# Kernel optimization log

Hardware: AMD Instinct MI355X
Metric: run time of the kernel (lower is better)

## Reference

```python
import jax, jax.numpy as jnp
import numpy as np

B, NPG, K, F_IN, H = 64, 256, 100, 5, 128  # graphs, nodes/graph, knn k, in feats, hidden
N = B * NPG
H2 = 6 * H
SLOPE = 0.01  # leaky_relu default
EPS = 1e-5    # batchnorm eps


def _leaky(x):
    return jnp.where(x > 0, x, SLOPE * x)


def _knn_edges(x):
    # knn_graph(x, K, batch), loop=False, flow=source_to_target: edges j->i for the
    # K nearest neighbors j of node i within the same graph.
    xb = x.reshape(B, NPG, F_IN)
    d2 = jnp.sum((xb[:, :, None, :] - xb[:, None, :, :]) ** 2, axis=-1)  # [B,NPG,NPG]
    d2 = d2 + jnp.eye(NPG, dtype=d2.dtype) * 1e10  # exclude self
    _, idx = jax.lax.top_k(-d2, K)  # [B,NPG,K] local neighbor ids
    offs = (jnp.arange(B) * NPG)[:, None, None]
    src = (idx + offs).reshape(-1)
    dst = jnp.broadcast_to(jnp.arange(NPG)[None, :, None] + offs, (B, NPG, K)).reshape(-1)
    return src, dst


def _tagconv(x, src, dst, norm, Ws, b):
    # PyG TAGConv: out = sum_k lin_k(L^k x), L = D^-1/2 A D^-1/2 (no self loops)
    out = x @ Ws[0]
    h = x
    for k in range(1, Ws.shape[0]):
        msg = h[src] * norm[:, None]                      # gather [E,F]
        h = jax.ops.segment_sum(msg, dst, num_segments=N)  # scatter-add
        out = out + h @ Ws[k]
    return out + b


def _pool(x, batch):
    cnt = jax.ops.segment_sum(jnp.ones((N,), x.dtype), batch, num_segments=B)
    mean = jax.ops.segment_sum(x, batch, num_segments=B) / cnt[:, None]
    mx = jax.ops.segment_max(x, batch, num_segments=B)
    return jnp.concatenate([mean, mx], axis=1)  # [B, 2F]


def reference(x, batch, conv1_w, conv1_b, conv2_w, conv2_b, conv3_w, conv3_b,
              bn_gamma, bn_beta, lin_w, lin_b, out_w, out_b):
    src, dst = _knn_edges(x)
    # gcn_norm: deg from target side, symmetric scaling
    deg = jax.ops.segment_sum(jnp.ones(src.shape, x.dtype), dst, num_segments=N)
    dinv = jnp.where(deg > 0, deg ** -0.5, 0.0)
    norm = dinv[src] * dinv[dst]

    h = _leaky(_tagconv(x, src, dst, norm, conv1_w, conv1_b))
    p1 = _pool(h, batch)
    h = _leaky(_tagconv(h, src, dst, norm, conv2_w, conv2_b))
    p2 = _pool(h, batch)
    h = _leaky(_tagconv(h, src, dst, norm, conv3_w, conv3_b))
    p3 = _pool(h, batch)

    g = jnp.concatenate([p1, p2, p3], axis=1)  # [B, 768]
    mu = jnp.mean(g, axis=0)
    var = jnp.mean((g - mu) ** 2, axis=0)
    g = (g - mu) * jax.lax.rsqrt(var + EPS) * bn_gamma + bn_beta

    for i in range(5):
        g = _leaky(g @ lin_w[i] + lin_b[i])
    return (g @ out_w + out_b).reshape(-1)


def setup_inputs() -> dict:
    key = jax.random.key(0)
    ks = jax.random.split(key, 16)
    x = jax.random.normal(ks[0], (N, F_IN), jnp.float32)
    batch = jnp.repeat(jnp.arange(B, dtype=jnp.int32), NPG)

    def w(k, shape, fan_in):
        return jax.random.normal(k, shape, jnp.float32) * (1.0 / np.sqrt(fan_in))

    return {
        "x": x, "batch": batch,
        "conv1_w": w(ks[1], (3, F_IN, H), F_IN), "conv1_b": jnp.zeros((H,), jnp.float32),
        "conv2_w": w(ks[2], (3, H, H), H), "conv2_b": jnp.zeros((H,), jnp.float32),
        "conv3_w": w(ks[3], (3, H, H), H), "conv3_b": jnp.zeros((H,), jnp.float32),
        "bn_gamma": jnp.ones((H2,), jnp.float32), "bn_beta": jnp.zeros((H2,), jnp.float32),
        "lin_w": w(ks[4], (5, H2, H2), H2), "lin_b": jnp.zeros((5, H2), jnp.float32),
        "out_w": w(ks[5], (H2, 1), H2), "out_b": jnp.zeros((1,), jnp.float32),
    }
```

## Files before the change

kernel.cpp:

```cpp
#include <hip/hip_runtime.h>
#include <hip/hip_bf16.h>
#include <math.h>

#define NN 16384
#define BB 64
#define NPG 256
#define KNN 100
#define FIN 5
#define HH 128
#define H2 768
#define SLOPE 0.01f

typedef __bf16 bf16x8 __attribute__((ext_vector_type(8)));
typedef float f32x4 __attribute__((ext_vector_type(4)));

__device__ __forceinline__ int detect_bf(const void* gamma) {
    return ((const unsigned*)gamma)[0] == 0x3F803F80u;
}
__device__ __forceinline__ float loadin(const void* p, size_t i, int bf) {
    return bf ? __bfloat162float(((const __hip_bfloat16*)p)[i]) : ((const float*)p)[i];
}
template <typename T>
__device__ __forceinline__ float ldT(const T* p, size_t i) { return (float)p[i]; }
template <>
__device__ __forceinline__ float ldT<__hip_bfloat16>(const __hip_bfloat16* p, size_t i) {
    return __bfloat162float(p[i]);
}
__device__ __forceinline__ float4 ldT4(const float* p) { return *(const float4*)p; }
__device__ __forceinline__ float4 ldT4(const __hip_bfloat16* p) {
    ushort4 u = *(const ushort4*)p;
    return make_float4(__uint_as_float((unsigned)u.x << 16),
                       __uint_as_float((unsigned)u.y << 16),
                       __uint_as_float((unsigned)u.z << 16),
                       __uint_as_float((unsigned)u.w << 16));
}
__device__ __forceinline__ void stage_chunk(float* dst, const float* src, int n, int t) {
    const float4* s = (const float4*)src;
    float4* d = (float4*)dst;
    int n4 = n >> 2;
    for (int i = t; i < n4; i += 256) d[i] = s[i];
}
__device__ __forceinline__ void stage_chunk(float* dst, const __hip_bfloat16* src, int n, int t) {
    const ushort4* s = (const ushort4*)src;
    int n4 = n >> 2;
    for (int i = t; i < n4; i += 256) {
        ushort4 u = s[i];
        dst[i * 4 + 0] = __uint_as_float((unsigned)u.x << 16);
        dst[i * 4 + 1] = __uint_as_float((unsigned)u.y << 16);
        dst[i * 4 + 2] = __uint_as_float((unsigned)u.z << 16);
        dst[i * 4 + 3] = __uint_as_float((unsigned)u.w << 16);
    }
}

__device__ __forceinline__ unsigned enc_f(float f) {
    unsigned u = __float_as_uint(f);
    return (u & 0x80000000u) ? ~u : (u | 0x80000000u);
}
__device__ __forceinline__ float dec_f(unsigned u) {
    return __uint_as_float((u & 0x80000000u) ? (u & 0x7FFFFFFFu) : ~u);
}
__device__ __forceinline__ unsigned f2bf(float f) {
    unsigned u = __float_as_uint(f);
    unsigned r = 0x7fffu + ((u >> 16) & 1u);
    return (u + r) >> 16;
}
__device__ __forceinline__ void split1(float x, unsigned short& h, unsigned short& l) {
    unsigned u = __float_as_uint(x);
    unsigned hb = u & 0xFFFF0000u;
    h = (unsigned short)(hb >> 16);
    float rem = x - __uint_as_float(hb);
    l = (unsigned short)f2bf(rem);
}

__global__ __launch_bounds__(256) void knn_kernel(const void* __restrict__ x_in,
                                                  const void* gamma,
                                                  unsigned char* __restrict__ nbr,
                                                  float* __restrict__ g,
                                                  float* __restrict__ outf,
                                                  unsigned* __restrict__ done) {
    int blk = blockIdx.x;
    int bf = detect_bf(gamma);
    int b = blk >> 6;
    int wave = threadIdx.x >> 6;
    int lane = threadIdx.x & 63;
    int il = ((blk & 63) << 2) + wave;
    {
        int gi = blk * 256 + threadIdx.x;
        if (blk < 192 && gi < BB * H2) {
            int cm = gi & 255;
            g[gi] = (cm < 128) ? 0.0f : __uint_as_float(0x007FFFFFu);
        }
        if (blk == 0 && threadIdx.x < BB) {
            outf[threadIdx.x] = 0.0f;
            done[threadIdx.x] = 0u;
        }
    }
    __shared__ float xg[FIN * NPG];
    for (int idx = threadIdx.x; idx < NPG * FIN; idx += 256) {
        int node = idx / FIN, c = idx - node * FIN;
        xg[c * NPG + node] = loadin(x_in, (size_t)b * NPG * FIN + idx, bf);
    }
    __syncthreads();
    float dq[4] = {0.f, 0.f, 0.f, 0.f};
    #pragma unroll
    for (int c = 0; c < FIN; ++c) {
        float xi = xg[c * NPG + il];
        float4 xv = *(const float4*)&xg[c * NPG + lane * 4];
        float d0 = xi - xv.x, d1 = xi - xv.y, d2 = xi - xv.z, d3 = xi - xv.w;
        dq[0] += d0 * d0; dq[1] += d1 * d1; dq[2] += d2 * d2; dq[3] += d3 * d3;
    }
    unsigned dk[4];
    #pragma unroll
    for (int q = 0; q < 4; ++q) {
        int e = lane * 4 + q;
        float dd = (e == il) ? 1e30f : dq[q];
        dk[q] = __float_as_uint(dd);
    }
    unsigned P = 0;
    for (int bit = 30; bit >= 0; --bit) {
        unsigned cand = P | (1u << bit);
        int c = __popcll(__ballot(dk[0] < cand)) + __popcll(__ballot(dk[1] < cand))
              + __popcll(__ballot(dk[2] < cand)) + __popcll(__ballot(dk[3] < cand));
        if (c < KNN) P = cand;
    }
    unsigned long long meq[4];
    int n_less = 0;
    #pragma unroll
    for (int q = 0; q < 4; ++q) {
        n_less += __popcll(__ballot(dk[q] < P));
        meq[q] = __ballot(dk[q] == P);
    }
    int quota = KNN - n_less;
    unsigned long long below = (1ull << lane) - 1ull;
    int run_eq = __popcll(meq[0] & below) + __popcll(meq[1] & below)
               + __popcll(meq[2] & below) + __popcll(meq[3] & below);
    bool sel[4];
    #pragma unroll
    for (int q = 0; q < 4; ++q) {
        int iseq = (int)((meq[q] >> lane) & 1ull);
        sel[q] = (dk[q] < P) || (iseq && run_eq < quota);
        run_eq += iseq;
    }
    unsigned long long msel[4];
    #pragma unroll
    for (int q = 0; q < 4; ++q) msel[q] = __ballot(sel[q]);
    int pos = __popcll(msel[0] & below) + __popcll(msel[1] & below)
            + __popcll(msel[2] & below) + __popcll(msel[3] & below);
    unsigned char* nb = &nbr[(size_t)(b * NPG + il) * KNN];
    #pragma unroll
    for (int q = 0; q < 4; ++q) {
        if (sel[q]) nb[pos] = (unsigned char)(lane * 4 + q);
        pos += sel[q] ? 1 : 0;
    }
}

__global__ void agg5x2_kernel(const void* __restrict__ x_in, const void* gamma,
                              const unsigned char* __restrict__ nbr,
                              float* __restrict__ t5a, float* __restrict__ t5b, float nrm) {
    int b = blockIdx.x, i = threadIdx.x;
    int bf = detect_bf(gamma);
    __shared__ float xs[NPG * FIN];
    __shared__ float ys[NPG * FIN];
    for (int idx = threadIdx.x; idx < NPG * FIN; idx += 256)
        xs[idx] = loadin(x_in, (size_t)b * NPG * FIN + idx, bf);
    __syncthreads();
    const unsigned char* nb = nbr + (size_t)(b * NPG + i) * KNN;
    float a0=0.f, a1=0.f, a2=0.f, a3=0.f, a4=0.f;
    for (int k = 0; k < KNN; ++k) {
        int base = (int)nb[k] * FIN;
        a0 += xs[base+0]; a1 += xs[base+1]; a2 += xs[base+2];
        a3 += xs[base+3]; a4 += xs[base+4];
    }
    a0 *= nrm; a1 *= nrm; a2 *= nrm; a3 *= nrm; a4 *= nrm;
    size_t o = (size_t)(b * NPG + i) * FIN;
    t5a[o+0] = a0; t5a[o+1] = a1; t5a[o+2] = a2; t5a[o+3] = a3; t5a[o+4] = a4;
    ys[i*FIN+0] = a0; ys[i*FIN+1] = a1; ys[i*FIN+2] = a2;
    ys[i*FIN+3] = a3; ys[i*FIN+4] = a4;
    __syncthreads();
    a0=0.f; a1=0.f; a2=0.f; a3=0.f; a4=0.f;
    for (int k = 0; k < KNN; ++k) {
        int base = (int)nb[k] * FIN;
        a0 += ys[base+0]; a1 += ys[base+1]; a2 += ys[base+2];
        a3 += ys[base+3]; a4 += ys[base+4];
    }
    t5b[o+0] = nrm*a0; t5b[o+1] = nrm*a1; t5b[o+2] = nrm*a2;
    t5b[o+3] = nrm*a3; t5b[o+4] = nrm*a4;
}

__global__ __launch_bounds__(256) void agg_mfma_kernel(
        const float* __restrict__ hin, const unsigned char* __restrict__ nbr,
        float* __restrict__ hout, float nrm) {
    __shared__ __align__(16) unsigned short At[64 * 256];
    __shared__ __align__(16) unsigned short Ht[64 * 256];
    int t = threadIdx.x;
    int gph = blockIdx.x;
    int m0 = blockIdx.y * 64;
    int c0 = blockIdx.z * 64;
    {
        uint4 zz = make_uint4(0u, 0u, 0u, 0u);
        uint4* za = (uint4*)At;
        #pragma unroll
        for (int i = 0; i < 8; ++i) za[t + i * 256] = zz;
    }
    __syncthreads();
    for (int it = t; it < NPG * 4; it += 256) {
        int nq = it >> 4, c4 = it & 15;
        const float* src = &hin[((size_t)(gph * NPG + nq * 4)) * HH + c0 + c4 * 4];
        float4 v0 = *(const float4*)(src);
        float4 v1 = *(const float4*)(src + HH);
        float4 v2 = *(const float4*)(src + 2 * HH);
        float4 v3 = *(const float4*)(src + 3 * HH);
        #pragma unroll
        for (int j = 0; j < 4; ++j) {
            int c = c4 * 4 + j;
            ushort4 pk;
            pk.x = (unsigned short)f2bf((&v0.x)[j]);
            pk.y = (unsigned short)f2bf((&v1.x)[j]);
            pk.z = (unsigned short)f2bf((&v2.x)[j]);
            pk.w = (unsigned short)f2bf((&v3.x)[j]);
            unsigned off = (unsigned)((c * 512 + nq * 8) ^ ((c & 7) << 4));
            *(ushort4*)((char*)Ht + off) = pk;
        }
    }
    {
        int r = t >> 2, q = t & 3;
        const unsigned char* nb = nbr + ((size_t)(gph * NPG + m0 + r)) * KNN + q * 25;
        unsigned rbase = (unsigned)(r * 512);
        unsigned rswz = (unsigned)((r & 7) << 4);
        for (int j = 0; j < 25; ++j) {
            int col = (int)nb[j];
            *(unsigned short*)((char*)At + ((rbase + col * 2) ^ rswz)) = 0x3F80u;
        }
    }
    __syncthreads();
    int wv = t >> 6, lane = t & 63;
    unsigned kgb = (unsigned)((lane >> 4) * 16);
    unsigned swz = (unsigned)((lane & 7) << 4);
    unsigned abase = (unsigned)((wv * 16 + (lane & 15)) * 512) + kgb;
    f32x4 acc[4];
    #pragma unroll
    for (int nt = 0; nt < 4; ++nt) acc[nt] = (f32x4){0.f, 0.f, 0.f, 0.f};
    #pragma unroll
    for (int ks = 0; ks < 8; ++ks) {
        bf16x8 a = *(const bf16x8*)((char*)At + ((abase + ks * 64) ^ swz));
        #pragma unroll
        for (int nt = 0; nt < 4; ++nt) {
            unsigned bb = (unsigned)((nt * 16 + (lane & 15)) * 512) + kgb + ks * 64;
            bf16x8 bv = *(const bf16x8*)((char*)Ht + (bb ^ swz));
            acc[nt] = __builtin_amdgcn_mfma_f32_16x16x32_bf16(a, bv, acc[nt], 0, 0, 0);
        }
    }
    int rbase2 = m0 + wv * 16 + (lane >> 4) * 4;
    #pragma unroll
    for (int nt = 0; nt < 4; ++nt) {
        int col = c0 + nt * 16 + (lane & 15);
        #pragma unroll
        for (int reg = 0; reg < 4; ++reg) {
            int node = gph * NPG + rbase2 + reg;
            hout[(size_t)node * HH + col] = acc[nt][reg] * nrm;
        }
    }
}

__device__ __forceinline__ void pool_epilogue(float* g, int b, int gc0, int cg, int rp,
                                              float* sv, float* mv) {
    #pragma unroll
    for (int mask = 1; mask < 16; mask <<= 1) {
        #pragma unroll
        for (int i = 0; i < 8; ++i) {
            sv[i] += __shfl_xor(sv[i], mask);
            mv[i] = fmaxf(mv[i], __shfl_xor(mv[i], mask));
        }
    }
    if (rp == 0) {
        #pragma unroll
        for (int i = 0; i < 8; ++i) {
            atomicAdd(&g[(size_t)b * H2 + gc0 + cg * 8 + i], sv[i]);
            atomicMax((unsigned*)&g[(size_t)b * H2 + gc0 + HH + cg * 8 + i], enc_f(mv[i]));
        }
    }
}

template <typename T>
__device__ __forceinline__ void tagmm5_body(
        const T* __restrict__ X0raw, const float* __restrict__ X1,
        const float* __restrict__ X2,
        const T* __restrict__ W, const T* __restrict__ bias,
        float* __restrict__ O, float* g, float* Ws, float* Xs) {
    int t = threadIdx.x;
    int r0 = blockIdx.x * 16;
    int r = t & 15, cg = t >> 4;
    float acc[8] = {0.f,0.f,0.f,0.f,0.f,0.f,0.f,0.f};
    for (int h = 0; h < 3; ++h) {
        stage_chunk(Ws, W + (size_t)h * FIN * HH, FIN * HH, t);
        for (int idx = t; idx < 16 * FIN; idx += 256) {
            int rr = idx / FIN, k = idx - rr * FIN;
            size_t src = (size_t)(r0 + rr) * FIN + k;
            Xs[rr * 9 + k] = (h == 0) ? ldT(X0raw, src)
                           : (h == 1) ? X1[src] : X2[src];
        }
        __syncthreads();
        #pragma unroll
        for (int k = 0; k < FIN; ++k) {
            float xv = Xs[r * 9 + k];
            const float4 wa = *(const float4*)&Ws[k * HH + cg * 8];
            const float4 wb = *(const float4*)&Ws[k * HH + cg * 8 + 4];
            acc[0] += xv * wa.x; acc[1] += xv * wa.y;
            acc[2] += xv * wa.z; acc[3] += xv * wa.w;
            acc[4] += xv * wb.x; acc[5] += xv * wb.y;
            acc[6] += xv * wb.z; acc[7] += xv * wb.w;
        }
        __syncthreads();
    }
    size_t orow = (size_t)(r0 + r) * HH + cg * 8;
    float sv[8], mv[8];
    #pragma unroll
    for (int m = 0; m < 8; ++m) {
        float v = acc[m] + ldT(bias, cg * 8 + m);
        v = v > 0.f ? v : SLOPE * v;
        O[orow + m] = v;
        sv[m] = v * (1.0f / NPG);
        mv[m] = v;
    }
    pool_epilogue(g, r0 >> 8, 0, cg, r, sv, mv);
}

__global__ __launch_bounds__(256) void tagmm5_kernel(
        const void* X0raw, const float* X1, const float* X2,
        const void* W, const void* bias, float* O, float* g, const void* gamma) {
    __shared__ float Ws[FIN * HH];
    __shared__ float Xs[16 * 9];
    if (detect_bf(gamma))
        tagmm5_body<__hip_bfloat16>((const __hip_bfloat16*)X0raw, X1, X2,
                                    (const __hip_bfloat16*)W,
                                    (const __hip_bfloat16*)bias, O, g, Ws, Xs);
    else
        tagmm5_body<float>((const float*)X0raw, X1, X2, (const float*)W,
                           (const float*)bias, O, g, Ws, Xs);
}

template <typename T>
__device__ __forceinline__ void tagmm_mfma_body(
        const float* __restrict__ X0, const float* __restrict__ X1,
        const float* __restrict__ X2,
        const T* __restrict__ W, const T* __restrict__ bias,
        float* __restrict__ O, float* g, int gcp,
        unsigned short* Xhi, unsigned short* Xlo,
        unsigned short* Whi, unsigned short* Wlo, float* pred) {
    int t = threadIdx.x;
    int m0 = blockIdx.x * 64;
    int gc0 = blockIdx.y * 64;
    int wv = t >> 6, lane = t & 63;
    const float* Xh[3] = {X0, X1, X2};
    f32x4 acc[4];
    #pragma unroll
    for (int nt = 0; nt < 4; ++nt) acc[nt] = (f32x4){0.f, 0.f, 0.f, 0.f};
    unsigned kgb = (unsigned)((lane >> 4) * 16);
    unsigned swz = (unsigned)((lane & 7) << 4);
    unsigned abase = (unsigned)((wv * 16 + (lane & 15)) * 256) + kgb;
    for (int h = 0; h < 3; ++h) {
        const float* X = Xh[h];
        for (int i = t; i < 2048; i += 256) {
            int row = i >> 5, c4 = i & 31;
            float4 v = *(const float4*)&X[(size_t)(m0 + row) * HH + c4 * 4];
            unsigned off = (unsigned)((row * 256 + c4 * 8) ^ ((row & 7) << 4));
            ushort4 h4, l4;
            split1(v.x, h4.x, l4.x); split1(v.y, h4.y, l4.y);
            split1(v.z, h4.z, l4.z); split1(v.w, h4.w, l4.w);
            *(ushort4*)((char*)Xhi + off) = h4;
            *(ushort4*)((char*)Xlo + off) = l4;
        }
        const T* Wg = W + ((size_t)h * HH) * HH + gc0;
        for (int i = t; i < 512; i += 256) {
            int kq = i >> 4, n4 = i & 15;
            int k0 = kq * 4;
            float4 v0 = ldT4(Wg + (size_t)(k0 + 0) * HH + n4 * 4);
            float4 v1 = ldT4(Wg + (size_t)(k0 + 1) * HH + n4 * 4);
            float4 v2 = ldT4(Wg + (size_t)(k0 + 2) * HH + n4 * 4);
            float4 v3 = ldT4(Wg + (size_t)(k0 + 3) * HH + n4 * 4);
            #pragma unroll
            for (int j = 0; j < 4; ++j) {
                int n = n4 * 4 + j;
                ushort4 hv, lv;
                split1((&v0.x)[j], hv.x, lv.x);
                split1((&v1.x)[j], hv.y, lv.y);
                split1((&v2.x)[j], hv.z, lv.z);
                split1((&v3.x)[j], hv.w, lv.w);
                unsigned off = (unsigned)((n * 256 + k0 * 2) ^ ((n & 7) << 4));
                *(ushort4*)((char*)Whi + off) = hv;
                *(ushort4*)((char*)Wlo + off) = lv;
            }
        }
        __syncthreads();
        #pragma unroll
        for (int ks = 0; ks < 4; ++ks) {
            bf16x8 ah = *(const bf16x8*)((char*)Xhi + ((abase + ks * 64) ^ swz));
            bf16x8 al = *(const bf16x8*)((char*)Xlo + ((abase + ks * 64) ^ swz));
            #pragma unroll
            for (int nt = 0; nt < 4; ++nt) {
                unsigned bb = ((unsigned)((nt * 16 + (lane & 15)) * 256) + kgb + ks * 64) ^ swz;
                bf16x8 bh = *(const bf16x8*)((char*)Whi + bb);
                bf16x8 bl = *(const bf16x8*)((char*)Wlo + bb);
                acc[nt] = __builtin_amdgcn_mfma_f32_16x16x32_bf16(ah, bh, acc[nt], 0, 0, 0);
                acc[nt] = __builtin_amdgcn_mfma_f32_16x16x32_bf16(ah, bl, acc[nt], 0, 0, 0);
                acc[nt] = __builtin_amdgcn_mfma_f32_16x16x32_bf16(al, bh, acc[nt], 0, 0, 0);
            }
        }
        __syncthreads();
    }
    int b = m0 >> 8;
    int grow0 = m0 + wv * 16 + (lane >> 4) * 4;
    float* psum = pred;
    float* pmax = pred + 256;
    #pragma unroll
    for (int nt = 0; nt < 4; ++nt) {
        int ncol = nt * 16 + (lane & 15);
        float bv = ldT(bias, gc0 + ncol);
        float cs = 0.f, cm = -INFINITY;
        #pragma unroll
        for (int reg = 0; reg < 4; ++reg) {
            float v = acc[nt][reg] + bv;
            v = v > 0.f ? v : SLOPE * v;
            O[(size_t)(grow0 + reg) * HH + gc0 + ncol] = v;
            cs += v;
            cm = fmaxf(cm, v);
        }
        cs += __shfl_xor(cs, 16); cs += __shfl_xor(cs, 32);
        cm = fmaxf(cm, __shfl_xor(cm, 16)); cm = fmaxf(cm, __shfl_xor(cm, 32));
        if (lane < 16) {
            psum[wv * 64 + ncol] = cs;
            pmax[wv * 64 + ncol] = cm;
        }
    }
    __syncthreads();
    if (t < 64) {
        float s = psum[t] + psum[64 + t] + psum[128 + t] + psum[192 + t];
        float m = fmaxf(fmaxf(pmax[t], pmax[64 + t]), fmaxf(pmax[128 + t], pmax[192 + t]));
        atomicAdd(&g[(size_t)b * H2 + gcp + gc0 + t], s * (1.0f / NPG));
        atomicMax((unsigned*)&g[(size_t)b * H2 + gcp + HH + gc0 + t], enc_f(m));
    }
}

__global__ __launch_bounds__(256) void tagmm_mfma_kernel(
        const float* X0, const float* X1, const float* X2,
        const void* W, const void* bias, float* O, float* g, int gcp, const void* gamma) {
    __shared__ __align__(16) unsigned short Xhi[64 * 128];
    __shared__ __align__(16) unsigned short Xlo[64 * 128];
    __shared__ __align__(16) unsigned short Whi[64 * 128];
    __shared__ __align__(16) unsigned short Wlo[64 * 128];
    __shared__ float pred[512];
    if (detect_bf(gamma))
        tagmm_mfma_body<__hip_bfloat16>(X0, X1, X2, (const __hip_bfloat16*)W,
                                        (const __hip_bfloat16*)bias, O, g, gcp,
                                        Xhi, Xlo, Whi, Wlo, pred);
    else
        tagmm_mfma_body<float>(X0, X1, X2, (const float*)W, (const float*)bias,
                               O, g, gcp, Xhi, Xlo, Whi, Wlo, pred);
}

__global__ void bn_split_kernel(const float* __restrict__ g, const void* gamma,
                                const void* beta, unsigned short* __restrict__ ghi,
                                unsigned short* __restrict__ glo) {
    int c = blockIdx.x * 128 + threadIdx.x;
    int bf = detect_bf(gamma);
    int ismax = (c & 255) >= 128;
    float s = 0.f, s2 = 0.f;
    #pragma unroll 8
    for (int b = 0; b < BB; ++b) {
        float raw = g[(size_t)b * H2 + c];
        float x = ismax ? dec_f(__float_as_uint(raw)) : raw;
        s += x; s2 += x * x;
    }
    float mu = s * (1.0f / BB);
    float var = fmaxf(s2 * (1.0f / BB) - mu * mu, 0.f);
    float rs = 1.0f / sqrtf(var + 1e-5f);
    float ga = loadin(gamma, c, bf), be = loadin(beta, c, bf);
    #pragma unroll 8
    for (int b = 0; b < BB; ++b) {
        float raw = g[(size_t)b * H2 + c];
        float x = ismax ? dec_f(__float_as_uint(raw)) : raw;
        float y = (x - mu) * rs * ga + be;
        unsigned short h, l;
        split1(y, h, l);
        ghi[(size_t)b * H2 + c] = h;
        glo[(size_t)b * H2 + c] = l;
    }
}

template <typename T>
__device__ __forceinline__ void mlp_mfma2_body(
        const unsigned short* __restrict__ Xhi_g, const unsigned short* __restrict__ Xlo_g,
        const T* __restrict__ W, const T* __restrict__ bias,
        unsigned short* __restrict__ Ohi, unsigned short* __restrict__ Olo,
        const T* __restrict__ ow, const T* __restrict__ ob,
        float* __restrict__ outf, unsigned* __restrict__ done, void* out, int bf,
        unsigned short* Xhi, unsigned short* Xlo,
        unsigned short* Whi, unsigned short* Wlo, float* red4, float* red) {
    int t = threadIdx.x;
    int col0 = blockIdx.x * 16;
    int wv = t >> 6, lane = t & 63;
    f32x4 acc[4];
    #pragma unroll
    for (int mt = 0; mt < 4; ++mt) acc[mt] = (f32x4){0.f, 0.f, 0.f, 0.f};
    unsigned swz = (unsigned)((lane & 7) << 4);
    unsigned kgb = (unsigned)(wv * 64 + (lane >> 4) * 16);
    for (int ch = 0; ch < 6; ++ch) {
        int k0 = ch * 128;
        #pragma unroll
        for (int u = 0; u < 4; ++u) {
            int i = t + u * 256;
            int row = i >> 4, grp = i & 15;
            uint4 vh = *(const uint4*)&Xhi_g[(size_t)row * H2 + k0 + grp * 8];
            uint4 vl = *(const uint4*)&Xlo_g[(size_t)row * H2 + k0 + grp * 8];
            unsigned off = (unsigned)((row * 256 + grp * 16) ^ ((row & 7) << 4));
            *(uint4*)((char*)Xhi + off) = vh;
            *(uint4*)((char*)Xlo + off) = vl;
        }
        if (t < 128) {
            int kq = t >> 2, n4 = t & 3;
            int kb = k0 + kq * 4;
            float4 v0 = ldT4(W + (size_t)(kb + 0) * H2 + col0 + n4 * 4);
            float4 v1 = ldT4(W + (size_t)(kb + 1) * H2 + col0 + n4 * 4);
            float4 v2 = ldT4(W + (size_t)(kb + 2) * H2 + col0 + n4 * 4);
            float4 v3 = ldT4(W + (size_t)(kb + 3) * H2 + col0 + n4 * 4);
            #pragma unroll
            for (int j = 0; j < 4; ++j) {
                int n = n4 * 4 + j;
                ushort4 hv, lv;
                split1((&v0.x)[j], hv.x, lv.x);
                split1((&v1.x)[j], hv.y, lv.y);
                split1((&v2.x)[j], hv.z, lv.z);
                split1((&v3.x)[j], hv.w, lv.w);
                unsigned off = (unsigned)((n * 256 + kq * 8) ^ ((n & 7) << 4));
                *(ushort4*)((char*)Whi + off) = hv;
                *(ushort4*)((char*)Wlo + off) = lv;
            }
        }
        __syncthreads();
        unsigned bb = ((unsigned)((lane & 15) * 256) + kgb) ^ swz;
        bf16x8 bh = *(const bf16x8*)((char*)Whi + bb);
        bf16x8 bl = *(const bf16x8*)((char*)Wlo + bb);
        #pragma unroll
        for (int mt = 0; mt < 4; ++mt) {
            unsigned ab = ((unsigned)((mt * 16 + (lane & 15)) * 256) + kgb) ^ swz;
            bf16x8 ah = *(const bf16x8*)((char*)Xhi + ab);
            bf16x8 al = *(const bf16x8*)((char*)Xlo + ab);
            acc[mt] = __builtin_amdgcn_mfma_f32_16x16x32_bf16(ah, bh, acc[mt], 0, 0, 0);
            acc[mt] = __builtin_amdgcn_mfma_f32_16x16x32_bf16(ah, bl, acc[mt], 0, 0, 0);
            acc[mt] = __builtin_amdgcn_mfma_f32_16x16x32_bf16(al, bh, acc[mt], 0, 0, 0);
            acc[mt] = __builtin_amdgcn_mfma_f32_16x16x32_bf16(al, bl, acc[mt], 0, 0, 0);
        }
        __syncthreads();
    }
    #pragma unroll
    for (int mt = 0; mt < 4; ++mt) {
        int row = mt * 16 + (lane >> 4) * 4;
        #pragma unroll
        for (int reg = 0; reg < 4; ++reg)
            red4[wv * 1024 + (row + reg) * 16 + (lane & 15)] = acc[mt][reg];
    }
    __syncthreads();
    int row = t >> 2, cq = t & 3;
    const float4 s0 = *(const float4*)&red4[t * 4];
    const float4 s1 = *(const float4*)&red4[1024 + t * 4];
    const float4 s2 = *(const float4*)&red4[2048 + t * 4];
    const float4 s3 = *(const float4*)&red4[3072 + t * 4];
    float vout[4];
    #pragma unroll
    for (int j = 0; j < 4; ++j) {
        float v = (&s0.x)[j] + (&s1.x)[j] + (&s2.x)[j] + (&s3.x)[j]
                + ldT(bias, col0 + cq * 4 + j);
        vout[j] = v > 0.f ? v : SLOPE * v;
    }
    if (Ohi) {
        ushort4 hv, lv;
        split1(vout[0], hv.x, lv.x); split1(vout[1], hv.y, lv.y);
        split1(vout[2], hv.z, lv.z); split1(vout[3], hv.w, lv.w);
        *(ushort4*)&Ohi[(size_t)row * H2 + col0 + cq * 4] = hv;
        *(ushort4*)&Olo[(size_t)row * H2 + col0 + cq * 4] = lv;
    } else {
        float p = 0.f;
        #pragma unroll
        for (int j = 0; j < 4; ++j)
            p += vout[j] * ldT(ow, col0 + cq * 4 + j);
        red[cq * 64 + row] = p;
        __syncthreads();
        if (t < BB) {
            float s = red[t] + red[64 + t] + red[128 + t] + red[192 + t];
            atomicAdd(&outf[t], s);
            __threadfence();
            unsigned ticket = atomicAdd(&done[t], 1u);
            if (ticket == 47u) {
                __threadfence();
                float v = outf[t] + ldT(ob, 0);
                if (bf) ((__hip_bfloat16*)out)[t] = __float2bfloat16(v);
                else    ((float*)out)[t] = v;
            }
        }
    }
}

__global__ __launch_bounds__(256) void mlp_mfma2_kernel(
        const unsigned short* Xhi_g, const unsigned short* Xlo_g,
        const void* W, size_t woff, const void* bias, size_t boff,
        unsigned short* Ohi, unsigned short* Olo,
        const void* ow, const void* ob, float* outf, unsigned* done, void* out,
        const void* gamma) {
    __shared__ __align__(16) unsigned short Xhi[64 * 128];
    __shared__ __align__(16) unsigned short Xlo[64 * 128];
    __shared__ __align__(16) unsigned short Whi[16 * 128];
    __shared__ __align__(16) unsigned short Wlo[16 * 128];
    __shared__ float red4[4 * 1024];
    __shared__ float red[256];
    if (detect_bf(gamma))
        mlp_mfma2_body<__hip_bfloat16>(Xhi_g, Xlo_g,
                                       (const __hip_bfloat16*)W + woff,
                                       (const __hip_bfloat16*)bias + boff, Ohi, Olo,
                                       (const __hip_bfloat16*)ow, (const __hip_bfloat16*)ob,
                                       outf, done, out, 1,
                                       Xhi, Xlo, Whi, Wlo, red4, red);
    else
        mlp_mfma2_body<float>(Xhi_g, Xlo_g, (const float*)W + woff,
                              (const float*)bias + boff, Ohi, Olo,
                              (const float*)ow, (const float*)ob,
                              outf, done, out, 0,
                              Xhi, Xlo, Whi, Wlo, red4, red);
}

extern "C" void kernel_launch(void* const* d_in, const int* in_sizes, int n_in,
                              void* d_out, int out_size, void* d_ws, size_t ws_size,
                              hipStream_t stream) {
    const void* x_in = d_in[0];
    const void* c1w = d_in[2];  const void* c1b = d_in[3];
    const void* c2w = d_in[4];  const void* c2b = d_in[5];
    const void* c3w = d_in[6];  const void* c3b = d_in[7];
    const void* gam = d_in[8];  const void* bet = d_in[9];
    const void* lw  = d_in[10]; const void* lb  = d_in[11];
    const void* ow  = d_in[12]; const void* obb = d_in[13];

    char* w = (char*)d_ws;
    unsigned char* nbr = (unsigned char*)w;  w += (size_t)NN * KNN;
    float* t5a = (float*)w;                  w += (size_t)NN * FIN * 4;
    float* t5b = (float*)w;                  w += (size_t)NN * FIN * 4;
    float* bufA = (float*)w;                 w += (size_t)NN * HH * 4;
    float* bufB = (float*)w;                 w += (size_t)NN * HH * 4;
    float* bufC = (float*)w;                 w += (size_t)NN * HH * 4;
    float* bufD = (float*)w;                 w += (size_t)NN * HH * 4;
    float* g = (float*)w;                    w += (size_t)BB * H2 * 4;
    float* mA = (float*)w;                   w += (size_t)BB * H2 * 4;
    float* mB = (float*)w;                   w += (size_t)BB * H2 * 4;
    float* outf = (float*)w;                 w += (size_t)BB * 4;
    unsigned* done = (unsigned*)w;           w += (size_t)BB * 4;
    unsigned short* Ahi = (unsigned short*)mA;
    unsigned short* Alo = Ahi + (size_t)BB * H2;
    unsigned short* Bhi = (unsigned short*)mB;
    unsigned short* Blo = Bhi + (size_t)BB * H2;

    float dinv = 1.0f / sqrtf((float)KNN);
    float nrm = dinv * dinv;

    knn_kernel<<<NN / 4, 256, 0, stream>>>(x_in, gam, nbr, g, outf, done);

    dim3 aggm_grid(BB, 4, 2);
    dim3 tag_grid(NN / 64, 2);

    agg5x2_kernel<<<BB, 256, 0, stream>>>(x_in, gam, nbr, t5a, t5b, nrm);
    tagmm5_kernel<<<NN / 16, 256, 0, stream>>>(x_in, t5a, t5b, c1w, c1b, bufA, g, gam);

    agg_mfma_kernel<<<aggm_grid, 256, 0, stream>>>(bufA, nbr, bufB, nrm);
    agg_mfma_kernel<<<aggm_grid, 256, 0, stream>>>(bufB, nbr, bufC, nrm);
    tagmm_mfma_kernel<<<tag_grid, 256, 0, stream>>>(bufA, bufB, bufC, c2w, c2b,
                                                    bufD, g, 256, gam);

    agg_mfma_kernel<<<aggm_grid, 256, 0, stream>>>(bufD, nbr, bufA, nrm);
    agg_mfma_kernel<<<aggm_grid, 256, 0, stream>>>(bufA, nbr, bufB, nrm);
    tagmm_mfma_kernel<<<tag_grid, 256, 0, stream>>>(bufD, bufA, bufB, c3w, c3b,
                                                    bufC, g, 512, gam);

    bn_split_kernel<<<6, 128, 0, stream>>>(g, gam, bet, Ahi, Alo);

    mlp_mfma2_kernel<<<48, 256, 0, stream>>>(Ahi, Alo, lw, (size_t)0 * H2 * H2,
                                             lb, 0 * H2, Bhi, Blo,
                                             nullptr, nullptr, nullptr, nullptr,
                                             nullptr, gam);
    mlp_mfma2_kernel<<<48, 256, 0, stream>>>(Bhi, Blo, lw, (size_t)1 * H2 * H2,
                                             lb, 1 * H2, Ahi, Alo,
                                             nullptr, nullptr, nullptr, nullptr,
                                             nullptr, gam);
    mlp_mfma2_kernel<<<48, 256, 0, stream>>>(Ahi, Alo, lw, (size_t)2 * H2 * H2,
                                             lb, 2 * H2, Bhi, Blo,
                                             nullptr, nullptr, nullptr, nullptr,
                                             nullptr, gam);
    mlp_mfma2_kernel<<<48, 256, 0, stream>>>(Bhi, Blo, lw, (size_t)3 * H2 * H2,
                                             lb, 3 * H2, Ahi, Alo,
                                             nullptr, nullptr, nullptr, nullptr,
                                             nullptr, gam);
    mlp_mfma2_kernel<<<48, 256, 0, stream>>>(Ahi, Alo, lw, (size_t)4 * H2 * H2,
                                             lb, 4 * H2, nullptr, nullptr,
                                             ow, obb, outf, done, d_out, gam);
}
```

Measured before the change: 264.1 us.

## Fuse two aggregation hops into one kernel with bitmask adjacency

Merges the two successive neighbor-aggregation launches per conv layer into one kernel. Each block now owns a whole graph for a 32-channel slice, keeps the first hop's result in shared memory as bf16, and feeds it straight into the second hop. The dense bf16 adjacency tile is replaced by a per-row 256-bit mask that is expanded into MFMA operands in registers, which cuts shared-memory zeroing and scattered stores. The cost is a smaller grid (256 blocks instead of 512 per hop pair) and the first-hop intermediate being rounded to bf16 before the second hop.

```diff
diff --git a/kernel.cpp b/kernel.cpp
--- a/kernel.cpp
+++ b/kernel.cpp
@@ -70,6 +70,14 @@
     h = (unsigned short)(hb >> 16);
     float rem = x - __uint_as_float(hb);
     l = (unsigned short)f2bf(rem);
+}
+__device__ __forceinline__ bf16x8 expand_bits(unsigned bits) {
+    uint4 aw;
+    aw.x = ((bits & 1u)   ? 0x3F80u : 0u) | ((bits & 2u)   ? 0x3F800000u : 0u);
+    aw.y = ((bits & 4u)   ? 0x3F80u : 0u) | ((bits & 8u)   ? 0x3F800000u : 0u);
+    aw.z = ((bits & 16u)  ? 0x3F80u : 0u) | ((bits & 32u)  ? 0x3F800000u : 0u);
+    aw.w = ((bits & 64u)  ? 0x3F80u : 0u) | ((bits & 128u) ? 0x3F800000u : 0u);
+    return *(bf16x8*)&aw;
 }
 
 __global__ __launch_bounds__(256) void knn_kernel(const void* __restrict__ x_in,
@@ -187,24 +195,31 @@
     t5b[o+3] = nrm*a3; t5b[o+4] = nrm*a4;
 }
 
-__global__ __launch_bounds__(256) void agg_mfma_kernel(
+__global__ __launch_bounds__(256) void agg2_mfma_kernel(
         const float* __restrict__ hin, const unsigned char* __restrict__ nbr,
-        float* __restrict__ hout, float nrm) {
-    __shared__ __align__(16) unsigned short At[64 * 256];
-    __shared__ __align__(16) unsigned short Ht[64 * 256];
+        float* __restrict__ hout1, float* __restrict__ hout2, float nrm) {
+    __shared__ unsigned Abits[256 * 9];
+    __shared__ __align__(16) unsigned short Ht[32 * 256];
+    __shared__ __align__(16) unsigned short H1t[32 * 256];
     int t = threadIdx.x;
     int gph = blockIdx.x;
-    int m0 = blockIdx.y * 64;
-    int c0 = blockIdx.z * 64;
+    int c0 = blockIdx.y * 32;
     {
-        uint4 zz = make_uint4(0u, 0u, 0u, 0u);
-        uint4* za = (uint4*)At;
-        #pragma unroll
-        for (int i = 0; i < 8; ++i) za[t + i * 256] = zz;
-    }
-    __syncthreads();
-    for (int it = t; it < NPG * 4; it += 256) {
-        int nq = it >> 4, c4 = it & 15;
+        unsigned m[8] = {0u,0u,0u,0u,0u,0u,0u,0u};
+        const unsigned char* nb = nbr + ((size_t)(gph * NPG + t)) * KNN;
+        #pragma unroll 5
+        for (int k4 = 0; k4 < KNN / 4; ++k4) {
+            uchar4 n4 = *(const uchar4*)&nb[k4 * 4];
+            m[n4.x >> 5] |= 1u << (n4.x & 31);
+            m[n4.y >> 5] |= 1u << (n4.y & 31);
+            m[n4.z >> 5] |= 1u << (n4.z & 31);
+            m[n4.w >> 5] |= 1u << (n4.w & 31);
+        }
+        #pragma unroll
+        for (int w = 0; w < 8; ++w) Abits[t * 9 + w] = m[w];
+    }
+    for (int it = t; it < NPG * 2; it += 256) {
+        int nq = it >> 3, c4 = it & 7;
         const float* src = &hin[((size_t)(gph * NPG + nq * 4)) * HH + c0 + c4 * 4];
         float4 v0 = *(const float4*)(src);
         float4 v1 = *(const float4*)(src + HH);
@@ -222,43 +237,50 @@
             *(ushort4*)((char*)Ht + off) = pk;
         }
     }
-    {
-        int r = t >> 2, q = t & 3;
-        const unsigned char* nb = nbr + ((size_t)(gph * NPG + m0 + r)) * KNN + q * 25;
-        unsigned rbase = (unsigned)(r * 512);
-        unsigned rswz = (unsigned)((r & 7) << 4);
-        for (int j = 0; j < 25; ++j) {
-            int col = (int)nb[j];
-            *(unsigned short*)((char*)At + ((rbase + col * 2) ^ rswz)) = 0x3F80u;
-        }
-    }
     __syncthreads();
     int wv = t >> 6, lane = t & 63;
-    unsigned kgb = (unsigned)((lane >> 4) * 16);
+    int kgrp = lane >> 4;
+    unsigned kgb = (unsigned)(kgrp * 16);
     unsigned swz = (unsigned)((lane & 7) << 4);
-    unsigned abase = (unsigned)((wv * 16 + (lane & 15)) * 512) + kgb;
-    f32x4 acc[4];
-    #pragma unroll
-    for (int nt = 0; nt < 4; ++nt) acc[nt] = (f32x4){0.f, 0.f, 0.f, 0.f};
-    #pragma unroll
-    for (int ks = 0; ks < 8; ++ks) {
-        bf16x8 a = *(const bf16x8*)((char*)At + ((abase + ks * 64) ^ swz));
-        #pragma unroll
-        for (int nt = 0; nt < 4; ++nt) {
-            unsigned bb = (unsigned)((nt * 16 + (lane & 15)) * 512) + kgb + ks * 64;
-            bf16x8 bv = *(const bf16x8*)((char*)Ht + (bb ^ swz));
-            acc[nt] = __builtin_amdgcn_mfma_f32_16x16x32_bf16(a, bv, acc[nt], 0, 0, 0);
-        }
-    }
-    int rbase2 = m0 + wv * 16 + (lane >> 4) * 4;
-    #pragma unroll
-    for (int nt = 0; nt < 4; ++nt) {
-        int col = c0 + nt * 16 + (lane & 15);
-        #pragma unroll
-        for (int reg = 0; reg < 4; ++reg) {
-            int node = gph * NPG + rbase2 + reg;
-            hout[(size_t)node * HH + col] = acc[nt][reg] * nrm;
-        }
+    #pragma unroll
+    for (int hop = 0; hop < 2; ++hop) {
+        const unsigned short* Bsrc = hop ? H1t : Ht;
+        float* gout = hop ? hout2 : hout1;
+        #pragma unroll
+        for (int mt = 0; mt < 4; ++mt) {
+            int rbase = wv * 64 + mt * 16;
+            int arow = rbase + (lane & 15);
+            f32x4 acc0 = (f32x4){0.f, 0.f, 0.f, 0.f};
+            f32x4 acc1 = (f32x4){0.f, 0.f, 0.f, 0.f};
+            #pragma unroll
+            for (int ks = 0; ks < 8; ++ks) {
+                unsigned bits = (Abits[arow * 9 + ks] >> (kgrp * 8)) & 0xFFu;
+                bf16x8 a = expand_bits(bits);
+                unsigned b0 = ((unsigned)((lane & 15) * 512) + kgb + ks * 64) ^ swz;
+                unsigned b1 = ((unsigned)((16 + (lane & 15)) * 512) + kgb + ks * 64) ^ swz;
+                bf16x8 bv0 = *(const bf16x8*)((char*)Bsrc + b0);
+                bf16x8 bv1 = *(const bf16x8*)((char*)Bsrc + b1);
+                acc0 = __builtin_amdgcn_mfma_f32_16x16x32_bf16(a, bv0, acc0, 0, 0, 0);
+                acc1 = __builtin_amdgcn_mfma_f32_16x16x32_bf16(a, bv1, acc1, 0, 0, 0);
+            }
+            int drow = rbase + (lane >> 4) * 4;
+            #pragma unroll
+            for (int nt = 0; nt < 2; ++nt) {
+                const f32x4& av = nt ? acc1 : acc0;
+                int ch = nt * 16 + (lane & 15);
+                #pragma unroll
+                for (int reg = 0; reg < 4; ++reg) {
+                    float v = av[reg] * nrm;
+                    gout[((size_t)(gph * NPG + drow + reg)) * HH + c0 + ch] = v;
+                    if (hop == 0) {
+                        unsigned off = ((unsigned)(ch * 512 + (drow + reg) * 2))
+                                     ^ ((unsigned)((ch & 7) << 4));
+                        *(unsigned short*)((char*)H1t + off) = (unsigned short)f2bf(v);
+                    }
+                }
+            }
+        }
+        __syncthreads();
     }
 }
 
@@ -661,19 +683,17 @@
 
     knn_kernel<<<NN / 4, 256, 0, stream>>>(x_in, gam, nbr, g, outf, done);
 
-    dim3 aggm_grid(BB, 4, 2);
+    dim3 agg2_grid(BB, 4);
     dim3 tag_grid(NN / 64, 2);
 
     agg5x2_kernel<<<BB, 256, 0, stream>>>(x_in, gam, nbr, t5a, t5b, nrm);
     tagmm5_kernel<<<NN / 16, 256, 0, stream>>>(x_in, t5a, t5b, c1w, c1b, bufA, g, gam);
 
-    agg_mfma_kernel<<<aggm_grid, 256, 0, stream>>>(bufA, nbr, bufB, nrm);
-    agg_mfma_kernel<<<aggm_grid, 256, 0, stream>>>(bufB, nbr, bufC, nrm);
+    agg2_mfma_kernel<<<agg2_grid, 256, 0, stream>>>(bufA, nbr, bufB, bufC, nrm);
     tagmm_mfma_kernel<<<tag_grid, 256, 0, stream>>>(bufA, bufB, bufC, c2w, c2b,
                                                     bufD, g, 256, gam);
 
-    agg_mfma_kernel<<<aggm_grid, 256, 0, stream>>>(bufD, nbr, bufA, nrm);
-    agg_mfma_kernel<<<aggm_grid, 256, 0, stream>>>(bufA, nbr, bufB, nrm);
+    agg2_mfma_kernel<<<agg2_grid, 256, 0, stream>>>(bufD, nbr, bufA, bufB, nrm);
     tagmm_mfma_kernel<<<tag_grid, 256, 0, stream>>>(bufD, bufA, bufB, c3w, c3b,
                                                     bufC, g, 512, gam);
 
```

Result: no change. 268.1 us (+1.5%).

## Compute first-layer 5-feature two-hop aggregation with bitmask adjacency and MFMA

Applied to the files above, without the earlier changes.

Replaces the scalar per-node gather-sum over 100 neighbours for the 5-feature input aggregation with a dense adjacency bitmask per graph, expanded to bf16 0/1 tiles and multiplied against hi/lo split bf16 features using MFMA. Both hops run in one kernel, with the first hop's result re-split into LDS for the second hop. This is meant to remove the serial, LDS-gather-bound loop of the old kernel. The cost is mostly wasted MFMA work, since only 5 of 16 columns are useful, plus bf16 hi/lo split precision.

```diff
diff --git a/kernel.cpp b/kernel.cpp
--- a/kernel.cpp
+++ b/kernel.cpp
@@ -70,6 +70,14 @@
     h = (unsigned short)(hb >> 16);
     float rem = x - __uint_as_float(hb);
     l = (unsigned short)f2bf(rem);
+}
+__device__ __forceinline__ bf16x8 expand_bits(unsigned bits) {
+    uint4 aw;
+    aw.x = ((bits & 1u)   ? 0x3F80u : 0u) | ((bits & 2u)   ? 0x3F800000u : 0u);
+    aw.y = ((bits & 4u)   ? 0x3F80u : 0u) | ((bits & 8u)   ? 0x3F800000u : 0u);
+    aw.z = ((bits & 16u)  ? 0x3F80u : 0u) | ((bits & 32u)  ? 0x3F800000u : 0u);
+    aw.w = ((bits & 64u)  ? 0x3F80u : 0u) | ((bits & 128u) ? 0x3F800000u : 0u);
+    return *(bf16x8*)&aw;
 }
 
 __global__ __launch_bounds__(256) void knn_kernel(const void* __restrict__ x_in,
@@ -154,37 +162,86 @@
     }
 }
 
-__global__ void agg5x2_kernel(const void* __restrict__ x_in, const void* gamma,
-                              const unsigned char* __restrict__ nbr,
-                              float* __restrict__ t5a, float* __restrict__ t5b, float nrm) {
-    int b = blockIdx.x, i = threadIdx.x;
+__global__ __launch_bounds__(256) void agg5x2_mfma_kernel(
+        const void* __restrict__ x_in, const void* gamma,
+        const unsigned char* __restrict__ nbr,
+        float* __restrict__ t5a, float* __restrict__ t5b, float nrm) {
+    __shared__ unsigned Abits[256 * 9];
+    __shared__ __align__(16) unsigned short Xhi[16 * 256];
+    __shared__ __align__(16) unsigned short Xlo[16 * 256];
+    __shared__ __align__(16) unsigned short H1hi[16 * 256];
+    __shared__ __align__(16) unsigned short H1lo[16 * 256];
+    int t = threadIdx.x;
+    int b = blockIdx.x;
     int bf = detect_bf(gamma);
-    __shared__ float xs[NPG * FIN];
-    __shared__ float ys[NPG * FIN];
-    for (int idx = threadIdx.x; idx < NPG * FIN; idx += 256)
-        xs[idx] = loadin(x_in, (size_t)b * NPG * FIN + idx, bf);
+    {
+        unsigned m[8] = {0u,0u,0u,0u,0u,0u,0u,0u};
+        const unsigned char* nb = nbr + ((size_t)(b * NPG + t)) * KNN;
+        #pragma unroll 5
+        for (int k4 = 0; k4 < KNN / 4; ++k4) {
+            uchar4 n4 = *(const uchar4*)&nb[k4 * 4];
+            m[n4.x >> 5] |= 1u << (n4.x & 31);
+            m[n4.y >> 5] |= 1u << (n4.y & 31);
+            m[n4.z >> 5] |= 1u << (n4.z & 31);
+            m[n4.w >> 5] |= 1u << (n4.w & 31);
+        }
+        #pragma unroll
+        for (int w = 0; w < 8; ++w) Abits[t * 9 + w] = m[w];
+    }
+    for (int idx = t; idx < NPG * FIN; idx += 256) {
+        int node = idx / FIN, c = idx - node * FIN;
+        float v = loadin(x_in, (size_t)b * NPG * FIN + idx, bf);
+        unsigned short h, l;
+        split1(v, h, l);
+        unsigned off = (unsigned)((c * 512 + node * 2) ^ ((c & 7) << 4));
+        *(unsigned short*)((char*)Xhi + off) = h;
+        *(unsigned short*)((char*)Xlo + off) = l;
+    }
     __syncthreads();
-    const unsigned char* nb = nbr + (size_t)(b * NPG + i) * KNN;
-    float a0=0.f, a1=0.f, a2=0.f, a3=0.f, a4=0.f;
-    for (int k = 0; k < KNN; ++k) {
-        int base = (int)nb[k] * FIN;
-        a0 += xs[base+0]; a1 += xs[base+1]; a2 += xs[base+2];
-        a3 += xs[base+3]; a4 += xs[base+4];
-    }
-    a0 *= nrm; a1 *= nrm; a2 *= nrm; a3 *= nrm; a4 *= nrm;
-    size_t o = (size_t)(b * NPG + i) * FIN;
-    t5a[o+0] = a0; t5a[o+1] = a1; t5a[o+2] = a2; t5a[o+3] = a3; t5a[o+4] = a4;
-    ys[i*FIN+0] = a0; ys[i*FIN+1] = a1; ys[i*FIN+2] = a2;
-    ys[i*FIN+3] = a3; ys[i*FIN+4] = a4;
-    __syncthreads();
-    a0=0.f; a1=0.f; a2=0.f; a3=0.f; a4=0.f;
-    for (int k = 0; k < KNN; ++k) {
-        int base = (int)nb[k] * FIN;
-        a0 += ys[base+0]; a1 += ys[base+1]; a2 += ys[base+2];
-        a3 += ys[base+3]; a4 += ys[base+4];
-    }
-    t5b[o+0] = nrm*a0; t5b[o+1] = nrm*a1; t5b[o+2] = nrm*a2;
-    t5b[o+3] = nrm*a3; t5b[o+4] = nrm*a4;
+    int wv = t >> 6, lane = t & 63;
+    int col = lane & 15;
+    int kgrp = lane >> 4;
+    unsigned kgb = (unsigned)(kgrp * 16);
+    unsigned swz = (unsigned)((lane & 7) << 4);
+    #pragma unroll
+    for (int hop = 0; hop < 2; ++hop) {
+        const unsigned short* Bhi_ = hop ? H1hi : Xhi;
+        const unsigned short* Blo_ = hop ? H1lo : Xlo;
+        float* gout = hop ? t5b : t5a;
+        #pragma unroll
+        for (int mt = 0; mt < 4; ++mt) {
+            int rbase = wv * 64 + mt * 16;
+            int arow = rbase + col;
+            f32x4 acc = (f32x4){0.f, 0.f, 0.f, 0.f};
+            #pragma unroll
+            for (int ks = 0; ks < 8; ++ks) {
+                unsigned bits = (Abits[arow * 9 + ks] >> (kgrp * 8)) & 0xFFu;
+                bf16x8 a = expand_bits(bits);
+                unsigned boff = ((unsigned)(col * 512) + kgb + (unsigned)(ks * 64)) ^ swz;
+                bf16x8 bh = *(const bf16x8*)((char*)Bhi_ + boff);
+                bf16x8 bl = *(const bf16x8*)((char*)Blo_ + boff);
+                acc = __builtin_amdgcn_mfma_f32_16x16x32_bf16(a, bh, acc, 0, 0, 0);
+                acc = __builtin_amdgcn_mfma_f32_16x16x32_bf16(a, bl, acc, 0, 0, 0);
+            }
+            if (col < FIN) {
+                int drow = rbase + (lane >> 4) * 4;
+                #pragma unroll
+                for (int reg = 0; reg < 4; ++reg) {
+                    float v = acc[reg] * nrm;
+                    gout[(size_t)(b * NPG + drow + reg) * FIN + col] = v;
+                    if (hop == 0) {
+                        unsigned short h, l;
+                        split1(v, h, l);
+                        unsigned off = (unsigned)((col * 512 + (drow + reg) * 2)
+                                                  ^ ((col & 7) << 4));
+                        *(unsigned short*)((char*)H1hi + off) = h;
+                        *(unsigned short*)((char*)H1lo + off) = l;
+                    }
+                }
+            }
+        }
+        __syncthreads();
+    }
 }
 
 __global__ __launch_bounds__(256) void agg_mfma_kernel(
@@ -664,7 +721,7 @@
     dim3 aggm_grid(BB, 4, 2);
     dim3 tag_grid(NN / 64, 2);
 
-    agg5x2_kernel<<<BB, 256, 0, stream>>>(x_in, gam, nbr, t5a, t5b, nrm);
+    agg5x2_mfma_kernel<<<BB, 256, 0, stream>>>(x_in, gam, nbr, t5a, t5b, nrm);
     tagmm5_kernel<<<NN / 16, 256, 0, stream>>>(x_in, t5a, t5b, c1w, c1b, bufA, g, gam);
 
     agg_mfma_kernel<<<aggm_grid, 256, 0, stream>>>(bufA, nbr, bufB, nrm);
```

Result: no change. 268.8 us (+1.8%).
